# Kernel optimization log

Measured on AMD Instinct MI355X. Metric: run time of the kernel, lower is better.

Reference implementation:

```python
import jax, jax.numpy as jnp
import numpy as np

L, B, IN, H, OUT = 4, 4096, 1024, 1024, 1024


def setup_inputs() -> dict:
    key = jax.random.key(0)
    ks = jax.random.split(key, 9)
    std = 1.0 / (H + IN) ** 0.5
    return {
        "x": jax.random.normal(ks[0], (B, IN), jnp.float32),
        "h_prev": jax.random.normal(ks[1], (L, B, H), jnp.float32),
        "c_prev": jax.random.normal(ks[2], (L, B, H), jnp.float32),
        "Wi": jax.random.uniform(ks[3], (L, IN, 4 * H), jnp.float32, -std, std),
        "Wh": jax.random.uniform(ks[4], (L, H, 4 * H), jnp.float32, -std, std),
        "bi": jax.random.uniform(ks[5], (L, 4 * H), jnp.float32, -std, std),
        "bh": jax.random.uniform(ks[6], (L, 4 * H), jnp.float32, -std, std),
        "fc_W": jax.random.uniform(ks[7], (H, OUT), jnp.float32, -std, std),
        "fc_b": jax.random.uniform(ks[8], (OUT,), jnp.float32, -std, std),
    }


def _lstm_cell(x, h, c, Wi, Wh, bi, bh):
    # gates: [B, 4H], split into (input, forget, cell, output)
    gates = x @ Wi + bi + h @ Wh + bh
    i, f, g, o = jnp.split(gates, 4, axis=1)
    i, f, o = jax.nn.sigmoid(i), jax.nn.sigmoid(f), jax.nn.sigmoid(o)
    g = jnp.tanh(g)
    c_cur = f * c + i * g
    h_cur = o * jnp.tanh(c_cur)
    return h_cur, c_cur


def reference(x, h_prev, c_prev, Wi, Wh, bi, bh, fc_W, fc_b):
    h_out, c_out = [], []
    x_in = x
    for l in range(L):  # fixed small layer loop
        h_cur, c_cur = _lstm_cell(x_in, h_prev[l], c_prev[l], Wi[l], Wh[l], bi[l], bh[l])
        h_out.append(h_cur)
        c_out.append(c_cur)
        x_in = h_cur
    h_out = jnp.stack(h_out, axis=0)
    c_out = jnp.stack(c_out, axis=0)
    y = h_out[-1] @ fc_W + fc_b
    return y, h_out, c_out
```

## Files before the change

kernel.cpp:

```cpp
#include <hip/hip_runtime.h>

#define B_    4096
#define H_    1024
#define NLAY  4

typedef __attribute__((ext_vector_type(8))) short bf16x8;
typedef __attribute__((ext_vector_type(4))) short s16x4;
typedef __attribute__((ext_vector_type(4))) float f32x4;
typedef unsigned short ushort_t;

__device__ __forceinline__ ushort_t f2bf(float f) {
  unsigned u = __builtin_bit_cast(unsigned, f);
  u += 0x7FFFu + ((u >> 16) & 1u);
  return (ushort_t)(u >> 16);
}

__device__ __forceinline__ float fast_sigmoid(float x) {
  float e = __expf(-fabsf(x));
  float s = 1.0f / (1.0f + e);
  return x >= 0.0f ? s : 1.0f - s;
}
__device__ __forceinline__ float fast_tanh(float x) {
  float e = __expf(-2.0f * fabsf(x));
  float t = (1.0f - e) / (1.0f + e);
  return x >= 0.0f ? t : -t;
}

#define GLDS16(gsrc, ldst)                                                  \
  __builtin_amdgcn_global_load_lds(                                         \
      (__attribute__((address_space(1))) void*)(gsrc),                      \
      (__attribute__((address_space(3))) void*)(ldst), 16, 0, 0)

#define BAR()                                                               \
  { asm volatile("" ::: "memory");                                          \
    __builtin_amdgcn_s_barrier();                                           \
    asm volatile("" ::: "memory"); }

#define WAITV(N)                                                            \
  { asm volatile("s_waitcnt vmcnt(" #N ")" ::: "memory");                   \
    __builtin_amdgcn_sched_barrier(0); }

__global__ __launch_bounds__(256, 2) void lstm8(
    const ushort_t* __restrict__ aX, const ushort_t* __restrict__ aH,
    const float* __restrict__ cprev, const float* __restrict__ bi,
    const float* __restrict__ bh, const ushort_t* __restrict__ wtl,
    float* __restrict__ hout, float* __restrict__ cout,
    ushort_t* __restrict__ hbfout) {
  __shared__ __align__(16) char sL[32768];

  const int tid  = threadIdx.x;
  const int lane = tid & 63;
  const int wid  = tid >> 6;
  const int bid  = (blockIdx.x & 7) * 64 + (blockIdx.x >> 3);
  const int bm   = bid & 31;
  const int bn   = bid >> 5;

  const int fr = lane & 15;
  const int oF = lane >> 4;
  const int aBase = fr * 64 + (oF ^ ((fr >> 1) & 3)) * 16;

  const int rowA = tid >> 2;
  const int oA   = (tid & 3) ^ ((rowA >> 1) & 3);
  const size_t aOff = (size_t)(bm * 128 + rowA) * 1024 + oA * 8;

  const ushort_t* wtBn = wtl + (size_t)bn * 524288;

  f32x4 acc[8][4];
#pragma unroll
  for (int m = 0; m < 8; ++m)
#pragma unroll
    for (int g = 0; g < 4; ++g) acc[m][g] = (f32x4){0.f, 0.f, 0.f, 0.f};

  bf16x8 bs0[4], bs1[4], bs2[4], bs3[4];

#define STAGE_A(NB, T)                                                       \
  {                                                                          \
    const ushort_t* s0 = (((T) < 32) ? aX : aH) + aOff + ((T) & 31) * 32;    \
    GLDS16(s0,         sL + (NB) * 8192 + wid * 1024);                       \
    GLDS16(s0 + 65536, sL + (NB) * 8192 + 4096 + wid * 1024);                \
  }
#define LOADB(SET, T)                                                        \
  {                                                                          \
    const ushort_t* b0 =                                                     \
        wtBn + ((size_t)(T) * 16 + wid * 4) * 512 + lane * 8;                \
    SET[0] = *(const bf16x8*)(b0);                                           \
    SET[1] = *(const bf16x8*)(b0 + 512);                                     \
    SET[2] = *(const bf16x8*)(b0 + 1024);                                    \
    SET[3] = *(const bf16x8*)(b0 + 1536);                                    \
  }

  STAGE_A(0, 0)
  LOADB(bs0, 0)
  STAGE_A(1, 1)
  LOADB(bs1, 1)
  STAGE_A(2, 2)
  WAITV(8)
  BAR()

#define TSTEP(CB, NB, T, BU, BL, IB, IA)                                     \
  {                                                                          \
    const char* pa = sL + (CB) * 8192;                                       \
    bf16x8 a[4];                                                             \
    _Pragma("unroll")                                                        \
    for (int m = 0; m < 4; ++m)                                              \
      a[m] = *(const bf16x8*)(pa + aBase + m * 1024);                        \
    if (IB) LOADB(BL, (T) + 2)                                               \
    __builtin_amdgcn_s_setprio(1);                                           \
    _Pragma("unroll")                                                        \
    for (int g = 0; g < 4; ++g)                                              \
      _Pragma("unroll")                                                      \
      for (int m = 0; m < 4; ++m)                                            \
        acc[m][g] = __builtin_amdgcn_mfma_f32_16x16x32_bf16(a[m], BU[g],     \
                                                            acc[m][g], 0, 0, 0); \
    __builtin_amdgcn_s_setprio(0);                                           \
    _Pragma("unroll")                                                        \
    for (int m = 0; m < 4; ++m)                                              \
      a[m] = *(const bf16x8*)(pa + aBase + 4096 + m * 1024);                 \
    if (IA) STAGE_A(NB, (T) + 3)                                             \
    __builtin_amdgcn_s_setprio(1);                                           \
    _Pragma("unroll")                                                        \
    for (int g = 0; g < 4; ++g)                                              \
      _Pragma("unroll")                                                      \
      for (int m = 0; m < 4; ++m)                                            \
        acc[m + 4][g] = __builtin_amdgcn_mfma_f32_16x16x32_bf16(              \
            a[m], BU[g], acc[m + 4][g], 0, 0, 0);                            \
    __builtin_amdgcn_s_setprio(0);                                           \
  }

#pragma unroll 1
  for (int t = 0; t < 60; t += 4) {
    TSTEP(0, 3, t + 0, bs0, bs2, 1, 1) WAITV(8) BAR()
    TSTEP(1, 0, t + 1, bs1, bs3, 1, 1) WAITV(8) BAR()
    TSTEP(2, 1, t + 2, bs2, bs0, 1, 1) WAITV(8) BAR()
    TSTEP(3, 2, t + 3, bs3, bs1, 1, 1) WAITV(8) BAR()
  }
  TSTEP(0, 3, 60, bs0, bs2, 1, 1) WAITV(8) BAR()
  TSTEP(1, 0, 61, bs1, bs3, 1, 0) WAITV(6) BAR()
  TSTEP(2, 1, 62, bs2, bs0, 0, 0) WAITV(0) BAR()
  TSTEP(3, 2, 63, bs3, bs0, 0, 0)
#undef TSTEP
#undef STAGE_A
#undef LOADB

  const int hcolL = wid * 16 + fr;
  const int hcol  = bn * 64 + hcolL;
  float bsum[4];
#pragma unroll
  for (int g = 0; g < 4; ++g)
    bsum[g] = bi[g * 1024 + hcol] + bh[g * 1024 + hcol];

  float* LF = (float*)sL;
  const int crow = tid >> 4;
  const int cc4  = (tid & 15) * 4;
  BAR()
  {
    const float* cp0 = cprev + (size_t)(bm * 128) * 1024 + bn * 64;
#pragma unroll
    for (int i = 0; i < 8; ++i) {
      const int row = i * 16 + crow;
      f32x4 v = *(const f32x4*)(cp0 + (size_t)row * 1024 + cc4);
      *(f32x4*)(LF + row * 64 + cc4) = v;
    }
  }
  BAR()
  float cv[8][4], hv[8][4];
#pragma unroll
  for (int m = 0; m < 8; ++m) {
    const int rowb = m * 16 + oF * 4;
#pragma unroll
    for (int r = 0; r < 4; ++r) {
      const float cp = LF[(rowb + r) * 64 + hcolL];
      const float gi = fast_sigmoid(acc[m][0][r] + bsum[0]);
      const float gf = fast_sigmoid(acc[m][1][r] + bsum[1]);
      const float gg = fast_tanh(acc[m][2][r] + bsum[2]);
      const float go = fast_sigmoid(acc[m][3][r] + bsum[3]);
      const float c  = gf * cp + gi * gg;
      cv[m][r] = c;
      hv[m][r] = go * fast_tanh(c);
    }
  }
  BAR()
#pragma unroll
  for (int m = 0; m < 8; ++m) {
    const int rowb = m * 16 + oF * 4;
#pragma unroll
    for (int r = 0; r < 4; ++r) LF[(rowb + r) * 64 + hcolL] = cv[m][r];
  }
  BAR()
  {
    float* co0 = cout + (size_t)(bm * 128) * 1024 + bn * 64;
#pragma unroll
    for (int i = 0; i < 8; ++i) {
      const int row = i * 16 + crow;
      f32x4 v = *(const f32x4*)(LF + row * 64 + cc4);
      *(f32x4*)(co0 + (size_t)row * 1024 + cc4) = v;
    }
  }
  BAR()
#pragma unroll
  for (int m = 0; m < 8; ++m) {
    const int rowb = m * 16 + oF * 4;
#pragma unroll
    for (int r = 0; r < 4; ++r) LF[(rowb + r) * 64 + hcolL] = hv[m][r];
  }
  BAR()
  {
    float* ho0 = hout + (size_t)(bm * 128) * 1024 + bn * 64;
    ushort_t* hb0 = hbfout + (size_t)(bm * 128) * 1024 + bn * 64;
#pragma unroll
    for (int i = 0; i < 8; ++i) {
      const int row = i * 16 + crow;
      f32x4 v = *(const f32x4*)(LF + row * 64 + cc4);
      *(f32x4*)(ho0 + (size_t)row * 1024 + cc4) = v;
      s16x4 hb;
#pragma unroll
      for (int j = 0; j < 4; ++j) hb[j] = (short)f2bf(v[j]);
      *(s16x4*)(hb0 + (size_t)row * 1024 + cc4) = hb;
    }
  }
}

__global__ __launch_bounds__(512) void packW(const float* __restrict__ Wi,
                                             const float* __restrict__ Wh,
                                             ushort_t* __restrict__ wt) {
  __shared__ ushort_t t16[64 * 256];
  const int bn = blockIdx.x;
  const int kb = blockIdx.y;
  const int l  = blockIdx.z;
  const int tid = threadIdx.x;
  const int kq = tid >> 6, cc = tid & 63;
  const int k0 = kb * 64;
  const float* W = (k0 < 1024)
                       ? (Wi + (size_t)l * 1024 * 4096 + (size_t)k0 * 4096)
                       : (Wh + (size_t)l * 1024 * 4096 + (size_t)(k0 - 1024) * 4096);
#pragma unroll
  for (int kk = 0; kk < 8; ++kk) {
    const int kl = kq * 8 + kk;
#pragma unroll
    for (int g = 0; g < 4; ++g) {
      const float v = W[(size_t)kl * 4096 + g * 1024 + bn * 64 + cc];
      const int p = (cc >> 4) * 64 + g * 16 + (cc & 15);
      t16[kl * 256 + p] = f2bf(v);
    }
  }
  __syncthreads();
#pragma unroll
  for (int half = 0; half < 2; ++half) {
    const int kt = kb * 2 + half;
    ushort_t* tile = wt + (((size_t)l * 16 + bn) * 64 + kt) * 8192;
#pragma unroll
    for (int c = 0; c < 2; ++c) {
      const int idx = c * 512 + tid;
      const int ln  = idx & 63;
      const int p   = (idx >> 6) * 16 + (ln & 15);
      const int klb = half * 32 + (ln >> 4) * 8;
      bf16x8 ov;
#pragma unroll
      for (int j = 0; j < 8; ++j) ov[j] = (short)t16[(klb + j) * 256 + p];
      *(bf16x8*)(tile + (size_t)idx * 8) = ov;
    }
  }
}

__device__ __forceinline__ int swz(int row, int kelem) {
  return ((row * 64 + kelem) * 2) ^ ((row & 7) << 4);
}

__global__ __launch_bounds__(512) void fc_kernel(
    const ushort_t* __restrict__ wtfc, const ushort_t* __restrict__ abf,
    const float* __restrict__ bias, float* __restrict__ y) {
  __shared__ __align__(16) char sA[128 * 64 * 2];
  __shared__ __align__(16) char sB[64 * 64 * 2];
  const int tid  = threadIdx.x;
  const int lane = tid & 63;
  const int wid  = tid >> 6;
  const int wm   = wid >> 2;
  const int wn   = wid & 3;
  const int bid  = (blockIdx.x & 7) * 64 + (blockIdx.x >> 3);
  const int bm   = bid & 31;
  const int bn   = bid >> 5;

  f32x4 acc[4];
#pragma unroll
  for (int m = 0; m < 4; ++m) acc[m] = (f32x4){0.f, 0.f, 0.f, 0.f};

  const int rloc = wid * 8 + (lane >> 3);
  const int jA   = (lane & 7) ^ ((lane >> 3) & 7);
  const ushort_t* aSrc = abf + (size_t)(bm * 128 + rloc) * 1024 + jA * 8;

  for (int ks = 0; ks < 16; ++ks) {
    __syncthreads();
    GLDS16(wtfc + (size_t)(bn * 16 + ks) * 4096 + tid * 8, sB + wid * 1024);
    const int off = ks * 64;
    GLDS16(aSrc + off,             sA + wid * 1024);
    GLDS16(aSrc + off + 64 * 1024, sA + 8192 + wid * 1024);
    __syncthreads();
#pragma unroll
    for (int kk = 0; kk < 64; kk += 32) {
      const int ke = kk + (lane >> 4) * 8;
      bf16x8 a[4];
#pragma unroll
      for (int m = 0; m < 4; ++m)
        a[m] = *(const bf16x8*)(sA + swz(wm * 64 + m * 16 + (lane & 15), ke));
      bf16x8 b = *(const bf16x8*)(sB + swz(wn * 16 + (lane & 15), ke));
#pragma unroll
      for (int m = 0; m < 4; ++m)
        acc[m] = __builtin_amdgcn_mfma_f32_16x16x32_bf16(a[m], b, acc[m], 0, 0, 0);
    }
  }
  const int col = bn * 64 + wn * 16 + (lane & 15);
  const float bb = bias[col];
#pragma unroll
  for (int m = 0; m < 4; ++m) {
    const int row0 = bm * 128 + wm * 64 + m * 16 + ((lane >> 4) << 2);
#pragma unroll
    for (int r = 0; r < 4; ++r)
      y[(size_t)(row0 + r) * 1024 + col] = acc[m][r] + bb;
  }
}

__global__ __launch_bounds__(512) void transposeFc(const float* __restrict__ W,
                                                   ushort_t* __restrict__ wt) {
  const int bn = blockIdx.x;
  const int ks = blockIdx.y;
  const int tid = threadIdx.x;
  const int c  = tid & 63;
  const int ko = (tid >> 6) * 8;
  float v[8];
#pragma unroll
  for (int j = 0; j < 8; ++j)
    v[j] = W[(size_t)(ks * 64 + ko + j) * 1024 + bn * 64 + c];
  bf16x8 o;
#pragma unroll
  for (int j = 0; j < 8; ++j) o[j] = (short)f2bf(v[j]);
  ushort_t* tile = wt + ((size_t)bn * 16 + ks) * 4096;
  *(bf16x8*)((char*)tile + swz(c, ko)) = o;
}

__global__ __launch_bounds__(256) void cvt_bf16(const float* __restrict__ s,
                                                ushort_t* __restrict__ d,
                                                int n8) {
  const int i = blockIdx.x * 256 + threadIdx.x;
  if (i >= n8) return;
  const float* p = s + (size_t)i * 8;
  f32x4 a = ((const f32x4*)p)[0];
  f32x4 b = ((const f32x4*)p)[1];
  bf16x8 o;
#pragma unroll
  for (int j = 0; j < 4; ++j) {
    o[j]     = (short)f2bf(a[j]);
    o[4 + j] = (short)f2bf(b[j]);
  }
  *(bf16x8*)(d + (size_t)i * 8) = o;
}

extern "C" void kernel_launch(void* const* d_in, const int* in_sizes, int n_in,
                              void* d_out, int out_size, void* d_ws,
                              size_t ws_size, hipStream_t stream) {
  const float* x     = (const float*)d_in[0];
  const float* hprev = (const float*)d_in[1];
  const float* cprev = (const float*)d_in[2];
  const float* Wi    = (const float*)d_in[3];
  const float* Wh    = (const float*)d_in[4];
  const float* bi    = (const float*)d_in[5];
  const float* bh    = (const float*)d_in[6];
  const float* fcW   = (const float*)d_in[7];
  const float* fcb   = (const float*)d_in[8];

  float* out = (float*)d_out;
  const size_t BH = (size_t)B_ * H_;
  float* y    = out;
  float* hout = out + BH;
  float* cout = out + 5 * BH;

  const size_t WT_ELEMS = (size_t)4 * 16 * 64 * 8192;
  const size_t FC_ELEMS = (size_t)16 * 16 * 4096;
  ushort_t* wt      = (ushort_t*)d_ws;
  ushort_t* fcwt    = wt + WT_ELEMS;
  ushort_t* xbf     = fcwt + FC_ELEMS;
  ushort_t* hprevbf = xbf + BH;
  ushort_t* houtbf  = hprevbf + 4 * BH;

  packW<<<dim3(16, 32, 4), dim3(512), 0, stream>>>(Wi, Wh, wt);
  transposeFc<<<dim3(16, 16), dim3(512), 0, stream>>>(fcW, fcwt);
  cvt_bf16<<<dim3((int)(BH / 8 / 256)), dim3(256), 0, stream>>>(x, xbf,
                                                                (int)(BH / 8));
  cvt_bf16<<<dim3((int)(4 * BH / 8 / 256)), dim3(256), 0, stream>>>(
      hprev, hprevbf, (int)(4 * BH / 8));

  for (int l = 0; l < NLAY; ++l) {
    const ushort_t* aX  = (l == 0) ? xbf : (houtbf + (size_t)(l - 1) * BH);
    const ushort_t* wtl = wt + (size_t)l * 16 * 64 * 8192;
    lstm8<<<dim3(512), dim3(256), 0, stream>>>(
        aX, hprevbf + (size_t)l * BH, cprev + (size_t)l * BH, bi + l * 4096,
        bh + l * 4096, wtl, hout + (size_t)l * BH, cout + (size_t)l * BH,
        houtbf + (size_t)l * BH);
  }
  fc_kernel<<<dim3(512), dim3(512), 0, stream>>>(fcwt, houtbf + 3 * BH, fcb, y);
}
```

Baseline: 431.2 us.

## Enlarge LSTM GEMM tile to 256x256 with LDS-staged weights and 8 waves

The LSTM gate GEMM kernel now uses 512-thread blocks, each computing a 256-row by 256-gate-column tile across a 2x4 wave grid. Weights are staged into shared memory with global_load_lds instead of being loaded straight into registers. The packed weight layout is rearranged into swizzled 64-deep K images to match, and the epilogue uses a padded LDS stride. The aim is more data reuse per block and fewer global weight reads. The cost is 128KB of LDS, one block per CU, only 256 blocks, and many barriers per K step.

```diff
diff --git a/kernel.cpp b/kernel.cpp
--- a/kernel.cpp
+++ b/kernel.cpp
@@ -40,29 +40,32 @@
   { asm volatile("s_waitcnt vmcnt(" #N ")" ::: "memory");                   \
     __builtin_amdgcn_sched_barrier(0); }
 
-__global__ __launch_bounds__(256, 2) void lstm8(
+__global__ __launch_bounds__(512, 1) void lstm8(
     const ushort_t* __restrict__ aX, const ushort_t* __restrict__ aH,
     const float* __restrict__ cprev, const float* __restrict__ bi,
     const float* __restrict__ bh, const ushort_t* __restrict__ wtl,
     float* __restrict__ hout, float* __restrict__ cout,
     ushort_t* __restrict__ hbfout) {
-  __shared__ __align__(16) char sL[32768];
+  __shared__ __align__(16) char sL[131072];
 
   const int tid  = threadIdx.x;
   const int lane = tid & 63;
   const int wid  = tid >> 6;
-  const int bid  = (blockIdx.x & 7) * 64 + (blockIdx.x >> 3);
-  const int bm   = bid & 31;
-  const int bn   = bid >> 5;
+  const int wm   = wid >> 2;
+  const int wn   = wid & 3;
+  const int bid  = (blockIdx.x & 7) * 32 + (blockIdx.x >> 3);
+  const int bm   = bid & 15;
+  const int bn   = bid >> 4;
 
   const int fr = lane & 15;
   const int oF = lane >> 4;
-  const int aBase = fr * 64 + (oF ^ ((fr >> 1) & 3)) * 16;
-
-  const int rowA = tid >> 2;
-  const int oA   = (tid & 3) ^ ((rowA >> 1) & 3);
-  const size_t aOff = (size_t)(bm * 128 + rowA) * 1024 + oA * 8;
-
+  const int sw = (oF ^ ((fr >> 1) & 3)) * 16;
+  const int aBase = wm * 16384 + fr * 64 + sw;
+  const int bBase = 65536 + (wn >> 1) * 16384 + (wn & 1) * 4096 + fr * 64 + sw;
+
+  const int oA = (tid & 3) ^ ((tid >> 3) & 3);
+  const size_t aOff0 = (size_t)(bm * 256 + (tid >> 2)) * 1024 + oA * 8;
+  const size_t aOff1 = aOff0 + (size_t)128 * 1024;
   const ushort_t* wtBn = wtl + (size_t)bn * 524288;
 
   f32x4 acc[8][4];
@@ -71,105 +74,141 @@
 #pragma unroll
     for (int g = 0; g < 4; ++g) acc[m][g] = (f32x4){0.f, 0.f, 0.f, 0.f};
 
-  bf16x8 bs0[4], bs1[4], bs2[4], bs3[4];
-
-#define STAGE_A(NB, T)                                                       \
+  bf16x8 ar[4][2], br0[2][2], br1[2][2];
+
+#define STAGE_A(PAR, HALF, TT)                                               \
   {                                                                          \
-    const ushort_t* s0 = (((T) < 32) ? aX : aH) + aOff + ((T) & 31) * 32;    \
-    GLDS16(s0,         sL + (NB) * 8192 + wid * 1024);                       \
-    GLDS16(s0 + 65536, sL + (NB) * 8192 + 4096 + wid * 1024);                \
-  }
-#define LOADB(SET, T)                                                        \
+    const ushort_t* s0 =                                                     \
+        (((TT) < 16) ? aX : aH) + ((HALF) ? aOff1 : aOff0) + ((TT) & 15) * 64; \
+    char* d = sL + (PAR) * 32768 + (HALF) * 16384 + wid * 1024;              \
+    GLDS16(s0, d);                                                           \
+    GLDS16(s0 + 32, d + 8192);                                               \
+  }
+#define STAGE_B(PAR, HALF, TT)                                               \
   {                                                                          \
-    const ushort_t* b0 =                                                     \
-        wtBn + ((size_t)(T) * 16 + wid * 4) * 512 + lane * 8;                \
-    SET[0] = *(const bf16x8*)(b0);                                           \
-    SET[1] = *(const bf16x8*)(b0 + 512);                                     \
-    SET[2] = *(const bf16x8*)(b0 + 1024);                                    \
-    SET[3] = *(const bf16x8*)(b0 + 1536);                                    \
-  }
-
-  STAGE_A(0, 0)
-  LOADB(bs0, 0)
-  STAGE_A(1, 1)
-  LOADB(bs1, 1)
-  STAGE_A(2, 2)
-  WAITV(8)
+    const ushort_t* s0 =                                                     \
+        wtBn + (size_t)((TT) & 31) * 16384 + (HALF) * 8192 + tid * 8;        \
+    char* d = sL + 65536 + (PAR) * 32768 + (HALF) * 16384 + wid * 1024;      \
+    GLDS16(s0, d);                                                           \
+    GLDS16(s0 + 4096, d + 8192);                                             \
+  }
+#define RD_A(PAR, MH)                                                        \
+  _Pragma("unroll") for (int mp = 0; mp < 4; ++mp)                           \
+      _Pragma("unroll") for (int kh = 0; kh < 2; ++kh)                       \
+      ar[mp][kh] = *(const bf16x8*)(sL + (PAR) * 32768 + kh * 8192 +         \
+                                    ((MH) * 4 + mp) * 1024 + aBase);
+#define RD_B(PAR, NH, BR)                                                    \
+  _Pragma("unroll") for (int gg = 0; gg < 2; ++gg)                           \
+      _Pragma("unroll") for (int kh = 0; kh < 2; ++kh)                       \
+      BR[gg][kh] = *(const bf16x8*)(sL + (PAR) * 32768 + kh * 8192 +         \
+                                    ((NH) * 2 + gg) * 1024 + bBase);
+#define MM(MH, NH, BR)                                                       \
+  __builtin_amdgcn_s_setprio(1);                                             \
+  _Pragma("unroll") for (int gg = 0; gg < 2; ++gg)                           \
+      _Pragma("unroll") for (int mp = 0; mp < 4; ++mp)                       \
+      _Pragma("unroll") for (int kh = 0; kh < 2; ++kh)                       \
+      acc[(MH) * 4 + mp][(NH) * 2 + gg] =                                    \
+          __builtin_amdgcn_mfma_f32_16x16x32_bf16(                           \
+              ar[mp][kh], BR[gg][kh], acc[(MH) * 4 + mp][(NH) * 2 + gg],     \
+              0, 0, 0);                                                      \
+  __builtin_amdgcn_s_setprio(0);
+
+  STAGE_A(0, 0, 0)
+  STAGE_A(0, 1, 0)
+  STAGE_B(0, 0, 0)
+  STAGE_B(0, 1, 0)
+  STAGE_B(1, 0, 1)
+  STAGE_B(1, 1, 1)
+  WAITV(4)
   BAR()
 
-#define TSTEP(CB, NB, T, BU, BL, IB, IA)                                     \
-  {                                                                          \
-    const char* pa = sL + (CB) * 8192;                                       \
-    bf16x8 a[4];                                                             \
-    _Pragma("unroll")                                                        \
-    for (int m = 0; m < 4; ++m)                                              \
-      a[m] = *(const bf16x8*)(pa + aBase + m * 1024);                        \
-    if (IB) LOADB(BL, (T) + 2)                                               \
-    __builtin_amdgcn_s_setprio(1);                                           \
-    _Pragma("unroll")                                                        \
-    for (int g = 0; g < 4; ++g)                                              \
-      _Pragma("unroll")                                                      \
-      for (int m = 0; m < 4; ++m)                                            \
-        acc[m][g] = __builtin_amdgcn_mfma_f32_16x16x32_bf16(a[m], BU[g],     \
-                                                            acc[m][g], 0, 0, 0); \
-    __builtin_amdgcn_s_setprio(0);                                           \
-    _Pragma("unroll")                                                        \
-    for (int m = 0; m < 4; ++m)                                              \
-      a[m] = *(const bf16x8*)(pa + aBase + 4096 + m * 1024);                 \
-    if (IA) STAGE_A(NB, (T) + 3)                                             \
-    __builtin_amdgcn_s_setprio(1);                                           \
-    _Pragma("unroll")                                                        \
-    for (int g = 0; g < 4; ++g)                                              \
-      _Pragma("unroll")                                                      \
-      for (int m = 0; m < 4; ++m)                                            \
-        acc[m + 4][g] = __builtin_amdgcn_mfma_f32_16x16x32_bf16(              \
-            a[m], BU[g], acc[m + 4][g], 0, 0, 0);                            \
-    __builtin_amdgcn_s_setprio(0);                                           \
-  }
-
 #pragma unroll 1
-  for (int t = 0; t < 60; t += 4) {
-    TSTEP(0, 3, t + 0, bs0, bs2, 1, 1) WAITV(8) BAR()
-    TSTEP(1, 0, t + 1, bs1, bs3, 1, 1) WAITV(8) BAR()
-    TSTEP(2, 1, t + 2, bs2, bs0, 1, 1) WAITV(8) BAR()
-    TSTEP(3, 2, t + 3, bs3, bs1, 1, 1) WAITV(8) BAR()
-  }
-  TSTEP(0, 3, 60, bs0, bs2, 1, 1) WAITV(8) BAR()
-  TSTEP(1, 0, 61, bs1, bs3, 1, 0) WAITV(6) BAR()
-  TSTEP(2, 1, 62, bs2, bs0, 0, 0) WAITV(0) BAR()
-  TSTEP(3, 2, 63, bs3, bs0, 0, 0)
-#undef TSTEP
+  for (int t2 = 0; t2 < 32; t2 += 2) {
+    RD_A(0, 0) RD_B(0, 0, br0)
+    STAGE_A(1, 0, t2 + 1)
+    BAR()
+    MM(0, 0, br0)
+    BAR()
+
+    RD_B(0, 1, br1)
+    STAGE_A(1, 1, t2 + 1)
+    BAR()
+    MM(0, 1, br1)
+    BAR()
+
+    RD_A(0, 1)
+    STAGE_B(0, 0, (t2 + 2))
+    BAR()
+    MM(1, 0, br0)
+    BAR()
+
+    STAGE_B(0, 1, (t2 + 2))
+    BAR()
+    MM(1, 1, br1)
+    WAITV(4)
+    BAR()
+
+    RD_A(1, 0) RD_B(1, 0, br0)
+    STAGE_A(0, 0, (t2 + 2))
+    BAR()
+    MM(0, 0, br0)
+    BAR()
+
+    RD_B(1, 1, br1)
+    STAGE_A(0, 1, (t2 + 2))
+    BAR()
+    MM(0, 1, br1)
+    BAR()
+
+    RD_A(1, 1)
+    STAGE_B(1, 0, (t2 + 3))
+    BAR()
+    MM(1, 0, br0)
+    BAR()
+
+    STAGE_B(1, 1, (t2 + 3))
+    BAR()
+    MM(1, 1, br1)
+    WAITV(4)
+    BAR()
+  }
 #undef STAGE_A
-#undef LOADB
-
-  const int hcolL = wid * 16 + fr;
+#undef STAGE_B
+#undef RD_A
+#undef RD_B
+#undef MM
+
+  WAITV(0)
+  __syncthreads();
+
+  const int hcolL = wn * 16 + fr;
   const int hcol  = bn * 64 + hcolL;
   float bsum[4];
 #pragma unroll
   for (int g = 0; g < 4; ++g)
     bsum[g] = bi[g * 1024 + hcol] + bh[g * 1024 + hcol];
 
+#define LSTRIDE 68
   float* LF = (float*)sL;
   const int crow = tid >> 4;
   const int cc4  = (tid & 15) * 4;
-  BAR()
   {
-    const float* cp0 = cprev + (size_t)(bm * 128) * 1024 + bn * 64;
+    const float* cp0 = cprev + (size_t)(bm * 256) * 1024 + bn * 64;
 #pragma unroll
     for (int i = 0; i < 8; ++i) {
-      const int row = i * 16 + crow;
+      const int row = i * 32 + crow;
       f32x4 v = *(const f32x4*)(cp0 + (size_t)row * 1024 + cc4);
-      *(f32x4*)(LF + row * 64 + cc4) = v;
-    }
-  }
-  BAR()
+      *(f32x4*)(LF + row * LSTRIDE + cc4) = v;
+    }
+  }
+  __syncthreads();
   float cv[8][4], hv[8][4];
 #pragma unroll
   for (int m = 0; m < 8; ++m) {
-    const int rowb = m * 16 + oF * 4;
+    const int rowb = wm * 128 + m * 16 + oF * 4;
 #pragma unroll
     for (int r = 0; r < 4; ++r) {
-      const float cp = LF[(rowb + r) * 64 + hcolL];
+      const float cp = LF[(rowb + r) * LSTRIDE + hcolL];
       const float gi = fast_sigmoid(acc[m][0][r] + bsum[0]);
       const float gf = fast_sigmoid(acc[m][1][r] + bsum[1]);
       const float gg = fast_tanh(acc[m][2][r] + bsum[2]);
@@ -179,38 +218,38 @@
       hv[m][r] = go * fast_tanh(c);
     }
   }
-  BAR()
+  __syncthreads();
 #pragma unroll
   for (int m = 0; m < 8; ++m) {
-    const int rowb = m * 16 + oF * 4;
-#pragma unroll
-    for (int r = 0; r < 4; ++r) LF[(rowb + r) * 64 + hcolL] = cv[m][r];
-  }
-  BAR()
+    const int rowb = wm * 128 + m * 16 + oF * 4;
+#pragma unroll
+    for (int r = 0; r < 4; ++r) LF[(rowb + r) * LSTRIDE + hcolL] = cv[m][r];
+  }
+  __syncthreads();
   {
-    float* co0 = cout + (size_t)(bm * 128) * 1024 + bn * 64;
+    float* co0 = cout + (size_t)(bm * 256) * 1024 + bn * 64;
 #pragma unroll
     for (int i = 0; i < 8; ++i) {
-      const int row = i * 16 + crow;
-      f32x4 v = *(const f32x4*)(LF + row * 64 + cc4);
+      const int row = i * 32 + crow;
+      f32x4 v = *(const f32x4*)(LF + row * LSTRIDE + cc4);
       *(f32x4*)(co0 + (size_t)row * 1024 + cc4) = v;
     }
   }
-  BAR()
+  __syncthreads();
 #pragma unroll
   for (int m = 0; m < 8; ++m) {
-    const int rowb = m * 16 + oF * 4;
-#pragma unroll
-    for (int r = 0; r < 4; ++r) LF[(rowb + r) * 64 + hcolL] = hv[m][r];
-  }
-  BAR()
+    const int rowb = wm * 128 + m * 16 + oF * 4;
+#pragma unroll
+    for (int r = 0; r < 4; ++r) LF[(rowb + r) * LSTRIDE + hcolL] = hv[m][r];
+  }
+  __syncthreads();
   {
-    float* ho0 = hout + (size_t)(bm * 128) * 1024 + bn * 64;
-    ushort_t* hb0 = hbfout + (size_t)(bm * 128) * 1024 + bn * 64;
+    float* ho0 = hout + (size_t)(bm * 256) * 1024 + bn * 64;
+    ushort_t* hb0 = hbfout + (size_t)(bm * 256) * 1024 + bn * 64;
 #pragma unroll
     for (int i = 0; i < 8; ++i) {
-      const int row = i * 16 + crow;
-      f32x4 v = *(const f32x4*)(LF + row * 64 + cc4);
+      const int row = i * 32 + crow;
+      f32x4 v = *(const f32x4*)(LF + row * LSTRIDE + cc4);
       *(f32x4*)(ho0 + (size_t)row * 1024 + cc4) = v;
       s16x4 hb;
 #pragma unroll
@@ -218,6 +257,7 @@
       *(s16x4*)(hb0 + (size_t)row * 1024 + cc4) = hb;
     }
   }
+#undef LSTRIDE
 }
 
 __global__ __launch_bounds__(512) void packW(const float* __restrict__ Wi,
@@ -225,11 +265,11 @@
                                              ushort_t* __restrict__ wt) {
   __shared__ ushort_t t16[64 * 256];
   const int bn = blockIdx.x;
-  const int kb = blockIdx.y;
+  const int T  = blockIdx.y;
   const int l  = blockIdx.z;
   const int tid = threadIdx.x;
   const int kq = tid >> 6, cc = tid & 63;
-  const int k0 = kb * 64;
+  const int k0 = T * 64;
   const float* W = (k0 < 1024)
                        ? (Wi + (size_t)l * 1024 * 4096 + (size_t)k0 * 4096)
                        : (Wh + (size_t)l * 1024 * 4096 + (size_t)(k0 - 1024) * 4096);
@@ -246,18 +286,21 @@
   __syncthreads();
 #pragma unroll
   for (int half = 0; half < 2; ++half) {
-    const int kt = kb * 2 + half;
-    ushort_t* tile = wt + (((size_t)l * 16 + bn) * 64 + kt) * 8192;
+    ushort_t* img =
+        wt + (((size_t)l * 16 + bn) * 32 + T) * 16384 + half * 8192;
 #pragma unroll
     for (int c = 0; c < 2; ++c) {
       const int idx = c * 512 + tid;
-      const int ln  = idx & 63;
-      const int p   = (idx >> 6) * 16 + (ln & 15);
-      const int klb = half * 32 + (ln >> 4) * 8;
+      const int kh = idx >> 9;
+      const int r  = (idx >> 2) & 127;
+      const int s  = idx & 3;
+      const int o  = s ^ ((r >> 1) & 3);
+      const int klb = kh * 32 + o * 8;
+      const int pg  = half * 128 + r;
       bf16x8 ov;
 #pragma unroll
-      for (int j = 0; j < 8; ++j) ov[j] = (short)t16[(klb + j) * 256 + p];
-      *(bf16x8*)(tile + (size_t)idx * 8) = ov;
+      for (int j = 0; j < 8; ++j) ov[j] = (short)t16[(klb + j) * 256 + pg];
+      *(bf16x8*)(img + (size_t)idx * 8) = ov;
     }
   }
 }
@@ -373,7 +416,7 @@
   float* hout = out + BH;
   float* cout = out + 5 * BH;
 
-  const size_t WT_ELEMS = (size_t)4 * 16 * 64 * 8192;
+  const size_t WT_ELEMS = (size_t)4 * 16 * 32 * 16384;
   const size_t FC_ELEMS = (size_t)16 * 16 * 4096;
   ushort_t* wt      = (ushort_t*)d_ws;
   ushort_t* fcwt    = wt + WT_ELEMS;
@@ -390,8 +433,8 @@
 
   for (int l = 0; l < NLAY; ++l) {
     const ushort_t* aX  = (l == 0) ? xbf : (houtbf + (size_t)(l - 1) * BH);
-    const ushort_t* wtl = wt + (size_t)l * 16 * 64 * 8192;
-    lstm8<<<dim3(512), dim3(256), 0, stream>>>(
+    const ushort_t* wtl = wt + (size_t)l * 16 * 32 * 16384;
+    lstm8<<<dim3(256), dim3(512), 0, stream>>>(
         aX, hprevbf + (size_t)l * BH, cprev + (size_t)l * BH, bi + l * 4096,
         bh + l * 4096, wtl, hout + (size_t)l * BH, cout + (size_t)l * BH,
         houtbf + (size_t)l * BH);
```

Measured after the change: 384.5 us. 10.8% less time.
